# Performance work log

Measured on AMD Instinct MI355X. Metric: run time of the kernel, lower is better.

The kernel has to match this reference:

```python
import jax, jax.numpy as jnp
import numpy as np

B, T, D_FEAT, FREQ, HID = 256, 128, 128, 16, 128


def setup_inputs() -> dict:
    key = jax.random.key(0)
    ks = jax.random.split(key, 14)
    n = lambda k, s, sc: jax.random.normal(k, s, jnp.float32) * sc
    sx = float(np.sqrt(2.0 / (D_FEAT + HID)))   # xavier-ish for W_*
    sf = float(np.sqrt(2.0 / (D_FEAT + FREQ)))
    sh = float(np.sqrt(1.0 / HID))              # stand-in for orthogonal U_*
    return {
        "input": jax.random.normal(ks[0], (B, D_FEAT * T), jnp.float32),
        "W_i": n(ks[1], (D_FEAT, HID), sx), "U_i": n(ks[2], (HID, HID), sh), "b_i": jnp.zeros((HID,), jnp.float32),
        "W_ste": n(ks[3], (D_FEAT, HID), sx), "U_ste": n(ks[4], (HID, HID), sh), "b_ste": jnp.ones((HID,), jnp.float32),
        "W_fre": n(ks[5], (D_FEAT, FREQ), sf), "U_fre": n(ks[6], (HID, FREQ), sh), "b_fre": jnp.ones((FREQ,), jnp.float32),
        "W_c": n(ks[7], (D_FEAT, HID), sx), "U_c": n(ks[8], (HID, HID), sh), "b_c": jnp.zeros((HID,), jnp.float32),
        "W_o": n(ks[9], (D_FEAT, HID), sx), "U_o": n(ks[10], (HID, HID), sh), "b_o": jnp.zeros((HID,), jnp.float32),
        "U_a": n(ks[11], (FREQ, 1), sh), "b_a": jnp.zeros((HID,), jnp.float32),
        "W_sym": n(ks[12], (HID, 1), sh), "b_sym": jnp.zeros((1,), jnp.float32),
    }


def _hsig(z):  # torch.nn.Hardsigmoid: relu6(x+3)/6
    return jnp.clip(z / 6.0 + 0.5, 0.0, 1.0)


def reference(input, W_i, U_i, b_i, W_ste, U_ste, b_ste, W_fre, U_fre, b_fre,
              W_c, U_c, b_c, W_o, U_o, b_o, U_a, b_a, W_sym, b_sym):
    Bsz = input.shape[0]
    x = input.reshape(Bsz, D_FEAT, -1).transpose(0, 2, 1)  # (B, T, D)
    # hoist the 5 input projections out of the time loop (identical math)
    xi = jnp.einsum('btd,dh->tbh', x, W_i) + b_i
    xste = jnp.einsum('btd,dh->tbh', x, W_ste) + b_ste
    xfre = jnp.einsum('btd,df->tbf', x, W_fre) + b_fre
    xc = jnp.einsum('btd,dh->tbh', x, W_c) + b_c
    xo = jnp.einsum('btd,dh->tbh', x, W_o) + b_o
    frequency = jnp.arange(FREQ, dtype=jnp.float32) / FREQ
    two_pi = jnp.float32(2.0 * np.pi)
    ua = U_a[:, 0]  # (FREQ,)

    def step(carry, xs):
        h, S_re, S_im, t = carry
        xi_t, xste_t, xfre_t, xc_t, xo_t = xs
        i = _hsig(xi_t + h @ U_i)
        ste = _hsig(xste_t + h @ U_ste)
        fre = _hsig(xfre_t + h @ U_fre)
        f = ste[:, :, None] * fre[:, None, :]          # (B, H, F)
        c = i * jnp.tanh(xc_t + h @ U_c)               # (B, H)
        t = t + 1.0
        omega = two_pi * t * frequency                 # (F,)
        S_re = f * S_re + c[:, :, None] * jnp.cos(omega)
        S_im = f * S_im + c[:, :, None] * jnp.sin(omega)
        A = S_re * S_re + S_im * S_im                  # (B, H, F)
        a = jnp.tanh(jnp.einsum('bhf,f->bh', A, ua) + b_a)
        o = _hsig(xo_t + h @ U_o)
        h = o * a
        return (h, S_re, S_im, t), None

    init = (jnp.zeros((Bsz, HID), jnp.float32),
            jnp.zeros((Bsz, HID, FREQ), jnp.float32),
            jnp.zeros((Bsz, HID, FREQ), jnp.float32),
            jnp.float32(0.0))
    (h, _, _, _), _ = jax.lax.scan(step, init, (xi, xste, xfre, xc, xo))
    return h @ W_sym + b_sym  # (B, num_symbols)
```

## Files before the change

### kernel.cpp

```cpp
#include <hip/hip_runtime.h>
#include <hip/hip_bf16.h>


__device__ __forceinline__ float hsig_f(float z) {
    return fminf(fmaxf(z * (1.0f / 6.0f) + 0.5f, 0.0f), 1.0f);
}

__global__ __launch_bounds__(256) void proj_gemm(
    const float* __restrict__ input,
    const float* __restrict__ Wi, const float* __restrict__ Wste,
    const float* __restrict__ Wc, const float* __restrict__ Wo,
    const float* __restrict__ Wfre,
    const float* __restrict__ bi, const float* __restrict__ bste,
    const float* __restrict__ bc, const float* __restrict__ bo,
    const float* __restrict__ bfre,
    float* __restrict__ P)
{
    __shared__ __align__(16) float XT[128 * 64];
    __shared__ __align__(16) float WT[128 * 64];

    const int ct = blockIdx.y;
    const float* W; const float* bias; int ncols, ccol0, cbase;
    if (ct < 2)      { W = Wi;   bias = bi;   ncols = 128; ccol0 = (ct & 1) * 64; cbase = ct * 64; }
    else if (ct < 4) { W = Wste; bias = bste; ncols = 128; ccol0 = (ct & 1) * 64; cbase = ct * 64; }
    else if (ct < 6) { W = Wc;   bias = bc;   ncols = 128; ccol0 = (ct & 1) * 64; cbase = ct * 64; }
    else if (ct < 8) { W = Wo;   bias = bo;   ncols = 128; ccol0 = (ct & 1) * 64; cbase = ct * 64; }
    else             { W = Wfre; bias = bfre; ncols = 16;  ccol0 = 0;             cbase = 512; }

    const int R  = blockIdx.x * 64;
    const int b  = R >> 7;
    const int t0 = R & 127;
    const int tid = threadIdx.x;

    const float* xbase = input + (size_t)b * 16384 + t0;
#pragma unroll
    for (int i = 0; i < 8; i++) {
        int flat4 = (i * 256 + tid) * 4;
        int rr = flat4 & 63, d = flat4 >> 6;
        float4 v = *(const float4*)(xbase + d * 128 + rr);
        *(float4*)(&XT[d * 64 + rr]) = v;
    }
#pragma unroll
    for (int i = 0; i < 8; i++) {
        int flat4 = (i * 256 + tid) * 4;
        int cc = flat4 & 63, d = flat4 >> 6;
        float4 v = make_float4(0.f, 0.f, 0.f, 0.f);
        if (cc < ncols) v = *(const float4*)(W + d * ncols + ccol0 + cc);
        *(float4*)(&WT[d * 64 + cc]) = v;
    }
    __syncthreads();

    const int tx = tid & 15, ty = tid >> 4;
    float acc[4][4] = {};
#pragma unroll 4
    for (int k = 0; k < 128; k++) {
        float4 xa = *(const float4*)(&XT[k * 64 + ty * 4]);
        float4 wb = *(const float4*)(&WT[k * 64 + tx * 4]);
        acc[0][0] = fmaf(xa.x, wb.x, acc[0][0]); acc[0][1] = fmaf(xa.x, wb.y, acc[0][1]);
        acc[0][2] = fmaf(xa.x, wb.z, acc[0][2]); acc[0][3] = fmaf(xa.x, wb.w, acc[0][3]);
        acc[1][0] = fmaf(xa.y, wb.x, acc[1][0]); acc[1][1] = fmaf(xa.y, wb.y, acc[1][1]);
        acc[1][2] = fmaf(xa.y, wb.z, acc[1][2]); acc[1][3] = fmaf(xa.y, wb.w, acc[1][3]);
        acc[2][0] = fmaf(xa.z, wb.x, acc[2][0]); acc[2][1] = fmaf(xa.z, wb.y, acc[2][1]);
        acc[2][2] = fmaf(xa.z, wb.z, acc[2][2]); acc[2][3] = fmaf(xa.z, wb.w, acc[2][3]);
        acc[3][0] = fmaf(xa.w, wb.x, acc[3][0]); acc[3][1] = fmaf(xa.w, wb.y, acc[3][1]);
        acc[3][2] = fmaf(xa.w, wb.z, acc[3][2]); acc[3][3] = fmaf(xa.w, wb.w, acc[3][3]);
    }

    const int colv = tx * 4;
    const bool valid = (ct < 8) || (colv < 16);
    if (valid) {
        float4 b4;
        b4.x = bias[ccol0 + colv + 0]; b4.y = bias[ccol0 + colv + 1];
        b4.z = bias[ccol0 + colv + 2]; b4.w = bias[ccol0 + colv + 3];
#pragma unroll
        for (int jr = 0; jr < 4; jr++) {
            int row = R + ty * 4 + jr;
            float4 o;
            o.x = acc[jr][0] + b4.x; o.y = acc[jr][1] + b4.y;
            o.z = acc[jr][2] + b4.z; o.w = acc[jr][3] + b4.w;
            *(float4*)(&P[(size_t)row * 528 + cbase + colv]) = o;
        }
    }
}

__global__ __launch_bounds__(512, 2) void recur_kernel(
    const float* __restrict__ P,
    const float* __restrict__ Ui, const float* __restrict__ Uste,
    const float* __restrict__ Uc, const float* __restrict__ Uo,
    const float* __restrict__ Ufre,
    const float* __restrict__ Ua, const float* __restrict__ ba_g,
    const float* __restrict__ Wsym, const float* __restrict__ bsym,
    float* __restrict__ out)
{
    __shared__ float ufre_lds[128 * 17];
    __shared__ float costab[16], sintab[16];
    __shared__ float gate_buf[512];
    __shared__ float fre_buf[16];
    __shared__ float h_buf[128];

    const int tid  = threadIdx.x;
    const int lane = tid & 63;
    const int wv   = tid >> 6;
    const int m    = tid >> 7;
    const int j    = tid & 127;
    const int hh   = tid >> 2;
    const int f0   = (tid & 3) * 4;
    const int b    = blockIdx.x;

    for (int e = tid; e < 2048; e += 512)
        ufre_lds[(e >> 4) * 17 + (e & 15)] = Ufre[e];
    if (tid < 16) {
        float ang = 6.283185307179586f * (float)tid * (1.0f / 16.0f);
        costab[tid] = cosf(ang);
        sintab[tid] = sinf(ang);
    }

    const float* Uptr = (m == 0) ? Ui : (m == 1) ? Uste : (m == 2) ? Uc : Uo;
    float Ucol[128];
#pragma unroll
    for (int k = 0; k < 128; k++) Ucol[k] = Uptr[k * 128 + j];

    float ua4[4];
#pragma unroll
    for (int q = 0; q < 4; q++) ua4[q] = Ua[f0 + q];
    const float ba = ba_g[hh];

    float hA = 0.0f, hB = 0.0f;
    float Sre0 = 0.f, Sre1 = 0.f, Sre2 = 0.f, Sre3 = 0.f;
    float Sim0 = 0.f, Sim1 = 0.f, Sim2 = 0.f, Sim3 = 0.f;
    int idx0 = 0, idx1 = 0, idx2 = 0, idx3 = 0;

    __syncthreads();

    const float* pr = P + (size_t)b * 128 * 528;
    for (int t = 0; t < 128; t++) {
        const float xpre  = pr[tid];
        const float xfrev = pr[512 + 2 * wv + (lane & 1)];

        float acc0 = 0.f, acc1 = 0.f;
#pragma unroll
        for (int kk = 0; kk < 64; kk++) {
            float s0 = __uint_as_float(__builtin_amdgcn_readlane(__float_as_uint(hA), kk));
            float s1 = __uint_as_float(__builtin_amdgcn_readlane(__float_as_uint(hB), kk));
            acc0 = fmaf(s0, Ucol[kk],      acc0);
            acc1 = fmaf(s1, Ucol[64 + kk], acc1);
        }
        float z = acc0 + acc1 + xpre;
        float g = (m == 2) ? tanhf(z) : hsig_f(z);
        gate_buf[tid] = g;

        {
            float u0 = ufre_lds[lane * 17 + 2 * wv];
            float u1 = ufre_lds[(64 + lane) * 17 + 2 * wv];
            float u2 = ufre_lds[lane * 17 + 2 * wv + 1];
            float u3 = ufre_lds[(64 + lane) * 17 + 2 * wv + 1];
            float p0 = fmaf(hA, u0, hB * u1);
            float p1 = fmaf(hA, u2, hB * u3);
#pragma unroll
            for (int off = 1; off <= 32; off <<= 1) {
                p0 += __shfl_xor(p0, off, 64);
                p1 += __shfl_xor(p1, off, 64);
            }
            float ps = (lane & 1) ? p1 : p0;
            float fv = hsig_f(ps + xfrev);
            if (lane < 2) fre_buf[2 * wv + lane] = fv;
        }
        __syncthreads();

        {
            float iv = gate_buf[hh];
            float sv = gate_buf[128 + hh];
            float tc = gate_buf[256 + hh];
            float ov = gate_buf[384 + hh];
            float c  = iv * tc;
            float aacc;

            idx0 = (idx0 + f0 + 0) & 15;
            idx1 = (idx1 + f0 + 1) & 15;
            idx2 = (idx2 + f0 + 2) & 15;
            idx3 = (idx3 + f0 + 3) & 15;

            float fc;
            fc = sv * fre_buf[f0 + 0];
            Sre0 = fmaf(fc, Sre0, c * costab[idx0]);
            Sim0 = fmaf(fc, Sim0, c * sintab[idx0]);
            aacc = fmaf(Sre0, Sre0, Sim0 * Sim0) * ua4[0];

            fc = sv * fre_buf[f0 + 1];
            Sre1 = fmaf(fc, Sre1, c * costab[idx1]);
            Sim1 = fmaf(fc, Sim1, c * sintab[idx1]);
            aacc = fmaf(fmaf(Sre1, Sre1, Sim1 * Sim1), ua4[1], aacc);

            fc = sv * fre_buf[f0 + 2];
            Sre2 = fmaf(fc, Sre2, c * costab[idx2]);
            Sim2 = fmaf(fc, Sim2, c * sintab[idx2]);
            aacc = fmaf(fmaf(Sre2, Sre2, Sim2 * Sim2), ua4[2], aacc);

            fc = sv * fre_buf[f0 + 3];
            Sre3 = fmaf(fc, Sre3, c * costab[idx3]);
            Sim3 = fmaf(fc, Sim3, c * sintab[idx3]);
            aacc = fmaf(fmaf(Sre3, Sre3, Sim3 * Sim3), ua4[3], aacc);

            aacc += __shfl_xor(aacc, 1, 64);
            aacc += __shfl_xor(aacc, 2, 64);
            if ((tid & 3) == 0) {
                float a = tanhf(aacc + ba);
                h_buf[hh] = ov * a;
            }
        }
        __syncthreads();
        hA = h_buf[lane];
        hB = h_buf[64 + lane];
        pr += 528;
    }

    if (wv == 0) {
        float v = fmaf(hA, Wsym[lane], hB * Wsym[64 + lane]);
#pragma unroll
        for (int off = 1; off <= 32; off <<= 1) v += __shfl_xor(v, off, 64);
        if (lane == 0) out[b] = v + bsym[0];
    }
}

extern "C" void kernel_launch(void* const* d_in, const int* in_sizes, int n_in,
                              void* d_out, int out_size, void* d_ws, size_t ws_size,
                              hipStream_t stream) {
    const float* input = (const float*)d_in[0];
    const float* W_i   = (const float*)d_in[1];
    const float* U_i   = (const float*)d_in[2];
    const float* b_i   = (const float*)d_in[3];
    const float* W_ste = (const float*)d_in[4];
    const float* U_ste = (const float*)d_in[5];
    const float* b_ste = (const float*)d_in[6];
    const float* W_fre = (const float*)d_in[7];
    const float* U_fre = (const float*)d_in[8];
    const float* b_fre = (const float*)d_in[9];
    const float* W_c   = (const float*)d_in[10];
    const float* U_c   = (const float*)d_in[11];
    const float* b_c   = (const float*)d_in[12];
    const float* W_o   = (const float*)d_in[13];
    const float* U_o   = (const float*)d_in[14];
    const float* b_o   = (const float*)d_in[15];
    const float* U_a   = (const float*)d_in[16];
    const float* b_a   = (const float*)d_in[17];
    const float* W_sym = (const float*)d_in[18];
    const float* b_sym = (const float*)d_in[19];

    float* P = (float*)d_ws;

    proj_gemm<<<dim3(512, 9), 256, 0, stream>>>(
        input, W_i, W_ste, W_c, W_o, W_fre,
        b_i, b_ste, b_c, b_o, b_fre, P);

    recur_kernel<<<256, 512, 0, stream>>>(
        P, U_i, U_ste, U_c, U_o, U_fre,
        U_a, b_a, W_sym, b_sym, (float*)d_out);
}
```

Before: 405.0 us.

## Restructure projection GEMM per batch and split recurrence K across 1024 threads

The projection GEMM now runs one block per batch row: the whole X tile stays in LDS and the kernel loops over the five weight matrices with a 4x8 register tile. The recurrent kernel doubles its block to 1024 threads. Each half of the block computes half of the K-range of h@U, and the partial sums are combined through LDS. The frequency gate is moved to the second half, and each thread keeps two frequency states instead of four. This is meant to shorten the serial per-step latency and the register pressure (64 U values instead of 128), at the cost of an extra barrier per step and lower parallelism in the GEMM grid.

New measurement: 382.9 us. 1.06x faster.

```diff
diff --git a/kernel.cpp b/kernel.cpp
--- a/kernel.cpp
+++ b/kernel.cpp
@@ -6,7 +6,7 @@
     return fminf(fmaxf(z * (1.0f / 6.0f) + 0.5f, 0.0f), 1.0f);
 }
 
-__global__ __launch_bounds__(256) void proj_gemm(
+__global__ __launch_bounds__(512) void proj_gemm(
     const float* __restrict__ input,
     const float* __restrict__ Wi, const float* __restrict__ Wste,
     const float* __restrict__ Wc, const float* __restrict__ Wo,
@@ -16,74 +16,85 @@
     const float* __restrict__ bfre,
     float* __restrict__ P)
 {
-    __shared__ __align__(16) float XT[128 * 64];
-    __shared__ __align__(16) float WT[128 * 64];
-
-    const int ct = blockIdx.y;
-    const float* W; const float* bias; int ncols, ccol0, cbase;
-    if (ct < 2)      { W = Wi;   bias = bi;   ncols = 128; ccol0 = (ct & 1) * 64; cbase = ct * 64; }
-    else if (ct < 4) { W = Wste; bias = bste; ncols = 128; ccol0 = (ct & 1) * 64; cbase = ct * 64; }
-    else if (ct < 6) { W = Wc;   bias = bc;   ncols = 128; ccol0 = (ct & 1) * 64; cbase = ct * 64; }
-    else if (ct < 8) { W = Wo;   bias = bo;   ncols = 128; ccol0 = (ct & 1) * 64; cbase = ct * 64; }
-    else             { W = Wfre; bias = bfre; ncols = 16;  ccol0 = 0;             cbase = 512; }
-
-    const int R  = blockIdx.x * 64;
-    const int b  = R >> 7;
-    const int t0 = R & 127;
+    __shared__ __align__(16) float XT[128 * 128];
+    __shared__ __align__(16) float WT[128 * 128];
+
+    const int b   = blockIdx.x;
     const int tid = threadIdx.x;
 
-    const float* xbase = input + (size_t)b * 16384 + t0;
+    const float* xb = input + (size_t)b * 16384;
 #pragma unroll
     for (int i = 0; i < 8; i++) {
-        int flat4 = (i * 256 + tid) * 4;
-        int rr = flat4 & 63, d = flat4 >> 6;
-        float4 v = *(const float4*)(xbase + d * 128 + rr);
-        *(float4*)(&XT[d * 64 + rr]) = v;
-    }
-#pragma unroll
-    for (int i = 0; i < 8; i++) {
-        int flat4 = (i * 256 + tid) * 4;
-        int cc = flat4 & 63, d = flat4 >> 6;
-        float4 v = make_float4(0.f, 0.f, 0.f, 0.f);
-        if (cc < ncols) v = *(const float4*)(W + d * ncols + ccol0 + cc);
-        *(float4*)(&WT[d * 64 + cc]) = v;
-    }
-    __syncthreads();
-
-    const int tx = tid & 15, ty = tid >> 4;
-    float acc[4][4] = {};
-#pragma unroll 4
-    for (int k = 0; k < 128; k++) {
-        float4 xa = *(const float4*)(&XT[k * 64 + ty * 4]);
-        float4 wb = *(const float4*)(&WT[k * 64 + tx * 4]);
-        acc[0][0] = fmaf(xa.x, wb.x, acc[0][0]); acc[0][1] = fmaf(xa.x, wb.y, acc[0][1]);
-        acc[0][2] = fmaf(xa.x, wb.z, acc[0][2]); acc[0][3] = fmaf(xa.x, wb.w, acc[0][3]);
-        acc[1][0] = fmaf(xa.y, wb.x, acc[1][0]); acc[1][1] = fmaf(xa.y, wb.y, acc[1][1]);
-        acc[1][2] = fmaf(xa.y, wb.z, acc[1][2]); acc[1][3] = fmaf(xa.y, wb.w, acc[1][3]);
-        acc[2][0] = fmaf(xa.z, wb.x, acc[2][0]); acc[2][1] = fmaf(xa.z, wb.y, acc[2][1]);
-        acc[2][2] = fmaf(xa.z, wb.z, acc[2][2]); acc[2][3] = fmaf(xa.z, wb.w, acc[2][3]);
-        acc[3][0] = fmaf(xa.w, wb.x, acc[3][0]); acc[3][1] = fmaf(xa.w, wb.y, acc[3][1]);
-        acc[3][2] = fmaf(xa.w, wb.z, acc[3][2]); acc[3][3] = fmaf(xa.w, wb.w, acc[3][3]);
-    }
-
-    const int colv = tx * 4;
-    const bool valid = (ct < 8) || (colv < 16);
-    if (valid) {
-        float4 b4;
-        b4.x = bias[ccol0 + colv + 0]; b4.y = bias[ccol0 + colv + 1];
-        b4.z = bias[ccol0 + colv + 2]; b4.w = bias[ccol0 + colv + 3];
-#pragma unroll
-        for (int jr = 0; jr < 4; jr++) {
-            int row = R + ty * 4 + jr;
-            float4 o;
-            o.x = acc[jr][0] + b4.x; o.y = acc[jr][1] + b4.y;
-            o.z = acc[jr][2] + b4.z; o.w = acc[jr][3] + b4.w;
-            *(float4*)(&P[(size_t)row * 528 + cbase + colv]) = o;
-        }
-    }
-}
-
-__global__ __launch_bounds__(512, 2) void recur_kernel(
+        int idx4 = (i * 512 + tid) * 4;
+        *(float4*)(&XT[idx4]) = *(const float4*)(xb + idx4);
+    }
+
+    const int tx   = tid & 15;
+    const int ty   = tid >> 4;
+    const int col0 = tx * 4;
+
+    const float* Ws[5]    = {Wi, Wste, Wc, Wo, Wfre};
+    const float* biases[5]= {bi, bste, bc, bo, bfre};
+
+    for (int ct = 0; ct < 5; ct++) {
+        const float* W = Ws[ct];
+        if (ct < 4) {
+#pragma unroll
+            for (int i = 0; i < 8; i++) {
+                int idx4 = (i * 512 + tid) * 4;
+                *(float4*)(&WT[idx4]) = *(const float4*)(W + idx4);
+            }
+        } else {
+            int idx4 = tid * 4;
+            if (idx4 < 2048) {
+                int d = idx4 >> 4, cc = idx4 & 15;
+                *(float4*)(&WT[d * 128 + cc]) = *(const float4*)(W + idx4);
+            }
+        }
+        __syncthreads();
+
+        float acc[4][8] = {};
+#pragma unroll 2
+        for (int k = 0; k < 128; k++) {
+            float4 xa = *(const float4*)(&XT[k * 128 + ty * 4]);
+            float4 w0 = *(const float4*)(&WT[k * 128 + col0]);
+            float4 w1 = *(const float4*)(&WT[k * 128 + 64 + col0]);
+            const float xr[4] = {xa.x, xa.y, xa.z, xa.w};
+            const float wc[8] = {w0.x, w0.y, w0.z, w0.w, w1.x, w1.y, w1.z, w1.w};
+#pragma unroll
+            for (int r = 0; r < 4; r++)
+#pragma unroll
+                for (int cc = 0; cc < 8; cc++)
+                    acc[r][cc] = fmaf(xr[r], wc[cc], acc[r][cc]);
+        }
+
+        const int cbase = (ct < 4) ? ct * 128 : 512;
+        const float* bias = biases[ct];
+#pragma unroll
+        for (int half = 0; half < 2; half++) {
+            int colg = half * 64 + col0;
+            bool valid = (ct < 4) || (colg < 16);
+            if (valid) {
+                float4 b4;
+                b4.x = bias[colg + 0]; b4.y = bias[colg + 1];
+                b4.z = bias[colg + 2]; b4.w = bias[colg + 3];
+#pragma unroll
+                for (int r = 0; r < 4; r++) {
+                    int row = b * 128 + ty * 4 + r;
+                    float4 o;
+                    o.x = acc[r][half * 4 + 0] + b4.x;
+                    o.y = acc[r][half * 4 + 1] + b4.y;
+                    o.z = acc[r][half * 4 + 2] + b4.z;
+                    o.w = acc[r][half * 4 + 3] + b4.w;
+                    *(float4*)(&P[(size_t)row * 528 + cbase + colg]) = o;
+                }
+            }
+        }
+        __syncthreads();
+    }
+}
+
+__global__ __launch_bounds__(1024) void recur_kernel(
     const float* __restrict__ P,
     const float* __restrict__ Ui, const float* __restrict__ Uste,
     const float* __restrict__ Uc, const float* __restrict__ Uo,
@@ -92,78 +103,78 @@
     const float* __restrict__ Wsym, const float* __restrict__ bsym,
     float* __restrict__ out)
 {
-    __shared__ float ufre_lds[128 * 17];
+    __shared__ float ufre_t[16 * 132];
     __shared__ float costab[16], sintab[16];
     __shared__ float gate_buf[512];
+    __shared__ float partial_buf[512];
     __shared__ float fre_buf[16];
     __shared__ float h_buf[128];
 
     const int tid  = threadIdx.x;
     const int lane = tid & 63;
-    const int wv   = tid >> 6;
-    const int m    = tid >> 7;
-    const int j    = tid & 127;
-    const int hh   = tid >> 2;
-    const int f0   = (tid & 3) * 4;
+    const int half = tid >> 9;
+    const int c    = tid & 511;
+    const int m    = c >> 7;
+    const int j    = c & 127;
+    const int hh   = tid >> 3;
+    const int fsel = tid & 7;
     const int b    = blockIdx.x;
 
-    for (int e = tid; e < 2048; e += 512)
-        ufre_lds[(e >> 4) * 17 + (e & 15)] = Ufre[e];
+    for (int e = tid; e < 2048; e += 1024) {
+        int k = e >> 4, col = e & 15;
+        ufre_t[col * 132 + k] = Ufre[e];
+    }
     if (tid < 16) {
         float ang = 6.283185307179586f * (float)tid * (1.0f / 16.0f);
         costab[tid] = cosf(ang);
         sintab[tid] = sinf(ang);
     }
+    if (tid < 128) h_buf[tid] = 0.0f;
 
     const float* Uptr = (m == 0) ? Ui : (m == 1) ? Uste : (m == 2) ? Uc : Uo;
-    float Ucol[128];
-#pragma unroll
-    for (int k = 0; k < 128; k++) Ucol[k] = Uptr[k * 128 + j];
-
-    float ua4[4];
-#pragma unroll
-    for (int q = 0; q < 4; q++) ua4[q] = Ua[f0 + q];
-    const float ba = ba_g[hh];
-
-    float hA = 0.0f, hB = 0.0f;
-    float Sre0 = 0.f, Sre1 = 0.f, Sre2 = 0.f, Sre3 = 0.f;
-    float Sim0 = 0.f, Sim1 = 0.f, Sim2 = 0.f, Sim3 = 0.f;
-    int idx0 = 0, idx1 = 0, idx2 = 0, idx3 = 0;
+    float Ucol[64];
+#pragma unroll
+    for (int k = 0; k < 64; k++) Ucol[k] = Uptr[(half * 64 + k) * 128 + j];
+
+    const float ua0 = Ua[fsel];
+    const float ua1 = Ua[fsel + 8];
+    const float ba  = ba_g[hh];
+
+    float hA = 0.0f;
+    float Sre0 = 0.f, Sim0 = 0.f, Sre1 = 0.f, Sim1 = 0.f;
+    int idx0 = 0, idx1 = 0;
 
     __syncthreads();
 
     const float* pr = P + (size_t)b * 128 * 528;
     for (int t = 0; t < 128; t++) {
-        const float xpre  = pr[tid];
-        const float xfrev = pr[512 + 2 * wv + (lane & 1)];
-
-        float acc0 = 0.f, acc1 = 0.f;
-#pragma unroll
-        for (int kk = 0; kk < 64; kk++) {
+        const float xpre = (half == 0) ? pr[c] : pr[512 + (c >> 5)];
+
+        float a0 = 0.f, a1 = 0.f;
+#pragma unroll
+        for (int kk = 0; kk < 64; kk += 2) {
             float s0 = __uint_as_float(__builtin_amdgcn_readlane(__float_as_uint(hA), kk));
-            float s1 = __uint_as_float(__builtin_amdgcn_readlane(__float_as_uint(hB), kk));
-            acc0 = fmaf(s0, Ucol[kk],      acc0);
-            acc1 = fmaf(s1, Ucol[64 + kk], acc1);
-        }
-        float z = acc0 + acc1 + xpre;
-        float g = (m == 2) ? tanhf(z) : hsig_f(z);
-        gate_buf[tid] = g;
-
-        {
-            float u0 = ufre_lds[lane * 17 + 2 * wv];
-            float u1 = ufre_lds[(64 + lane) * 17 + 2 * wv];
-            float u2 = ufre_lds[lane * 17 + 2 * wv + 1];
-            float u3 = ufre_lds[(64 + lane) * 17 + 2 * wv + 1];
-            float p0 = fmaf(hA, u0, hB * u1);
-            float p1 = fmaf(hA, u2, hB * u3);
-#pragma unroll
-            for (int off = 1; off <= 32; off <<= 1) {
-                p0 += __shfl_xor(p0, off, 64);
-                p1 += __shfl_xor(p1, off, 64);
-            }
-            float ps = (lane & 1) ? p1 : p0;
-            float fv = hsig_f(ps + xfrev);
-            if (lane < 2) fre_buf[2 * wv + lane] = fv;
+            float s1 = __uint_as_float(__builtin_amdgcn_readlane(__float_as_uint(hA), kk + 1));
+            a0 = fmaf(s0, Ucol[kk],     a0);
+            a1 = fmaf(s1, Ucol[kk + 1], a1);
+        }
+        float acc = a0 + a1;
+
+        if (half) partial_buf[c] = acc;
+        __syncthreads();
+
+        if (half == 0) {
+            float z = acc + partial_buf[c] + xpre;
+            float g = (m == 2) ? tanhf(z) : hsig_f(z);
+            gate_buf[c] = g;
+        } else {
+            const int col = c >> 5, kg = c & 31;
+            float4 hv = *(const float4*)(&h_buf[kg * 4]);
+            float4 uv = *(const float4*)(&ufre_t[col * 132 + kg * 4]);
+            float p = fmaf(hv.x, uv.x, fmaf(hv.y, uv.y, fmaf(hv.z, uv.z, hv.w * uv.w)));
+#pragma unroll
+            for (int off = 1; off <= 16; off <<= 1) p += __shfl_xor(p, off, 64);
+            if (kg == 0) fre_buf[col] = hsig_f(p + xpre);
         }
         __syncthreads();
 
@@ -172,50 +183,35 @@
             float sv = gate_buf[128 + hh];
             float tc = gate_buf[256 + hh];
             float ov = gate_buf[384 + hh];
-            float c  = iv * tc;
-            float aacc;
-
-            idx0 = (idx0 + f0 + 0) & 15;
-            idx1 = (idx1 + f0 + 1) & 15;
-            idx2 = (idx2 + f0 + 2) & 15;
-            idx3 = (idx3 + f0 + 3) & 15;
-
-            float fc;
-            fc = sv * fre_buf[f0 + 0];
-            Sre0 = fmaf(fc, Sre0, c * costab[idx0]);
-            Sim0 = fmaf(fc, Sim0, c * sintab[idx0]);
-            aacc = fmaf(Sre0, Sre0, Sim0 * Sim0) * ua4[0];
-
-            fc = sv * fre_buf[f0 + 1];
-            Sre1 = fmaf(fc, Sre1, c * costab[idx1]);
-            Sim1 = fmaf(fc, Sim1, c * sintab[idx1]);
-            aacc = fmaf(fmaf(Sre1, Sre1, Sim1 * Sim1), ua4[1], aacc);
-
-            fc = sv * fre_buf[f0 + 2];
-            Sre2 = fmaf(fc, Sre2, c * costab[idx2]);
-            Sim2 = fmaf(fc, Sim2, c * sintab[idx2]);
-            aacc = fmaf(fmaf(Sre2, Sre2, Sim2 * Sim2), ua4[2], aacc);
-
-            fc = sv * fre_buf[f0 + 3];
-            Sre3 = fmaf(fc, Sre3, c * costab[idx3]);
-            Sim3 = fmaf(fc, Sim3, c * sintab[idx3]);
-            aacc = fmaf(fmaf(Sre3, Sre3, Sim3 * Sim3), ua4[3], aacc);
-
+            float cg = iv * tc;
+
+            idx0 = (idx0 + fsel) & 15;
+            idx1 = (idx1 + fsel + 8) & 15;
+
+            float f0v = sv * fre_buf[fsel];
+            float f1v = sv * fre_buf[fsel + 8];
+            Sre0 = fmaf(f0v, Sre0, cg * costab[idx0]);
+            Sim0 = fmaf(f0v, Sim0, cg * sintab[idx0]);
+            Sre1 = fmaf(f1v, Sre1, cg * costab[idx1]);
+            Sim1 = fmaf(f1v, Sim1, cg * sintab[idx1]);
+
+            float aacc = fmaf(Sre0, Sre0, Sim0 * Sim0) * ua0;
+            aacc = fmaf(fmaf(Sre1, Sre1, Sim1 * Sim1), ua1, aacc);
             aacc += __shfl_xor(aacc, 1, 64);
             aacc += __shfl_xor(aacc, 2, 64);
-            if ((tid & 3) == 0) {
+            aacc += __shfl_xor(aacc, 4, 64);
+            if (fsel == 0) {
                 float a = tanhf(aacc + ba);
                 h_buf[hh] = ov * a;
             }
         }
         __syncthreads();
-        hA = h_buf[lane];
-        hB = h_buf[64 + lane];
+        hA = h_buf[half * 64 + lane];
         pr += 528;
     }
 
-    if (wv == 0) {
-        float v = fmaf(hA, Wsym[lane], hB * Wsym[64 + lane]);
+    if (tid < 64) {
+        float v = fmaf(h_buf[lane], Wsym[lane], h_buf[64 + lane] * Wsym[64 + lane]);
 #pragma unroll
         for (int off = 1; off <= 32; off <<= 1) v += __shfl_xor(v, off, 64);
         if (lane == 0) out[b] = v + bsym[0];
@@ -248,11 +244,11 @@
 
     float* P = (float*)d_ws;
 
-    proj_gemm<<<dim3(512, 9), 256, 0, stream>>>(
+    proj_gemm<<<256, 512, 0, stream>>>(
         input, W_i, W_ste, W_c, W_o, W_fre,
         b_i, b_ste, b_c, b_o, b_fre, P);
 
-    recur_kernel<<<256, 512, 0, stream>>>(
+    recur_kernel<<<256, 1024, 0, stream>>>(
         P, U_i, U_ste, U_c, U_o, U_fre,
         U_a, b_a, W_sym, b_sym, (float*)d_out);
 }
```
